# Performance work log

Hardware: AMD Instinct MI355X
Metric: run time of the kernel (lower is better)

The kernel has to match this reference:

```python
import jax, jax.numpy as jnp
import numpy as np

B, S, H, NH = 4, 2048, 1024, 16
HD = H // NH  # head dim 64


def setup_inputs() -> dict:
    key = jax.random.key(0)
    ks = jax.random.split(key, 8)
    s = 1.0 / np.sqrt(H)
    return {
        "hidden_states": jax.random.normal(ks[0], (B, S, H), dtype=jnp.float32),
        "attention_mask": jnp.zeros((B, 1, 1, S), dtype=jnp.float32),
        "Wq": jax.random.normal(ks[1], (H, H), dtype=jnp.float32) * s,
        "bq": jnp.zeros((H,), dtype=jnp.float32),
        "Wk": jax.random.normal(ks[2], (H, H), dtype=jnp.float32) * s,
        "bk": jnp.zeros((H,), dtype=jnp.float32),
        "Wv": jax.random.normal(ks[3], (H, H), dtype=jnp.float32) * s,
        "bv": jnp.zeros((H,), dtype=jnp.float32),
    }


def _split_heads(x):
    # [B,S,H] -> [B,NH,S,HD]
    b, s, _ = x.shape
    return x.reshape(b, s, NH, HD).transpose(0, 2, 1, 3)


def reference(hidden_states, attention_mask, Wq, bq, Wk, bk, Wv, bv):
    q = _split_heads(hidden_states @ Wq.T + bq)
    k = _split_heads(hidden_states @ Wk.T + bk)
    v = _split_heads(hidden_states @ Wv.T + bv)

    qk = jnp.einsum("bhid,bhjd->bhij", q, k)  # [B,NH,S,S]
    seq = q.shape[2]
    causal = jnp.triu(jnp.ones((seq, seq), dtype=bool), 1)  # True above diagonal
    attn_w = jnp.where(causal, -jnp.inf, qk) + attention_mask
    # NOTE: original divides by sqrt(d_k) AFTER masking/adding attention_mask
    probs = jax.nn.softmax(attn_w / jnp.sqrt(jnp.float32(HD)), axis=-1)
    out = jnp.einsum("bhij,bhjd->bhid", probs, v)  # [B,NH,S,HD]
    return out.transpose(0, 2, 1, 3).reshape(hidden_states.shape[0], seq, NH * HD)
```

## Files before the change

### kernel.cpp

```cpp
#include <hip/hip_runtime.h>


#define B_   4
#define S_   2048
#define H_   1024
#define NH_  16
#define HD_  64
#define M_   (B_ * S_)

typedef float          f32x4  __attribute__((ext_vector_type(4)));
typedef short          bf16x8 __attribute__((ext_vector_type(8)));
typedef unsigned short u16x8  __attribute__((ext_vector_type(8)));

__device__ __forceinline__ unsigned short f2bf(float f) {
    unsigned int u = __float_as_uint(f);
    u += 0x7fffu + ((u >> 16) & 1u);
    return (unsigned short)(u >> 16);
}

__device__ __forceinline__ void load16_lds(const unsigned short* g, unsigned short* l) {
    __builtin_amdgcn_global_load_lds(
        (const __attribute__((address_space(1))) unsigned int*)g,
        (__attribute__((address_space(3))) unsigned int*)l, 16, 0, 0);
}

__global__ __launch_bounds__(256) void cast_bf16(
    const float* __restrict__ s0, const float* __restrict__ s1,
    const float* __restrict__ s2, const float* __restrict__ s3,
    unsigned short* __restrict__ d0, unsigned short* __restrict__ d1,
    unsigned short* __restrict__ d2, unsigned short* __restrict__ d3) {
    const int z = blockIdx.y;
    const float* src = (z == 0) ? s0 : (z == 1) ? s1 : (z == 2) ? s2 : s3;
    unsigned short* dst = (z == 0) ? d0 : (z == 1) ? d1 : (z == 2) ? d2 : d3;
    const int n = (z == 0) ? M_ * H_ : H_ * H_;
    int i = (blockIdx.x * 256 + threadIdx.x) * 8;
    if (i + 8 <= n) {
        float4 a = *(const float4*)(src + i);
        float4 b = *(const float4*)(src + i + 4);
        u16x8 o;
        o[0] = f2bf(a.x); o[1] = f2bf(a.y); o[2] = f2bf(a.z); o[3] = f2bf(a.w);
        o[4] = f2bf(b.x); o[5] = f2bf(b.y); o[6] = f2bf(b.z); o[7] = f2bf(b.w);
        *(u16x8*)(dst + i) = o;
    }
}

__global__ __launch_bounds__(256) void qkv_gemm(
    const unsigned short* __restrict__ A,
    const unsigned short* __restrict__ W0, const unsigned short* __restrict__ W1,
    const unsigned short* __restrict__ W2,
    const float* __restrict__ b0, const float* __restrict__ b1,
    const float* __restrict__ b2,
    unsigned short* __restrict__ o0, unsigned short* __restrict__ o1,
    unsigned short* __restrict__ o2) {
    __shared__ unsigned short sA[128 * 64];
    __shared__ unsigned short sB[128 * 64];
    __shared__ unsigned short sT[64 * 136];

    const int t = threadIdx.x;
    const int w = t >> 6, lane = t & 63, quad = lane >> 4, l15 = lane & 15;
    const int bm = blockIdx.x, bn = blockIdx.y, z = blockIdx.z;

    const unsigned short* W = (z == 0) ? W0 : (z == 1) ? W1 : W2;
    const float*        bia = (z == 0) ? b0 : (z == 1) ? b1 : b2;

    const int wm = (w & 1) * 64, wn = (w >> 1) * 64;

    f32x4 acc[4][4];
#pragma unroll
    for (int i = 0; i < 4; ++i)
#pragma unroll
        for (int j = 0; j < 4; ++j) acc[i][j] = f32x4{0.f, 0.f, 0.f, 0.f};

    const int srow = w * 32 + (lane >> 3);
    const int scol = (lane & 7) * 8;
    const unsigned short* Ag = A + (size_t)(bm * 128 + srow) * H_ + scol;
    const unsigned short* Wg = W + (size_t)(bn * 128 + srow) * H_ + scol;
    unsigned short* lA = &sA[w * 32 * 64];
    unsigned short* lB = &sB[w * 32 * 64];

    for (int kt = 0; kt < 16; ++kt) {
        __syncthreads();
#pragma unroll
        for (int c = 0; c < 4; ++c) {
            load16_lds(Ag + kt * 64 + (size_t)c * 8 * H_, lA + c * 512);
            load16_lds(Wg + kt * 64 + (size_t)c * 8 * H_, lB + c * 512);
        }
        __syncthreads();
#pragma unroll
        for (int kk = 0; kk < 64; kk += 32) {
            bf16x8 af[4], bf[4];
#pragma unroll
            for (int mi = 0; mi < 4; ++mi)
                af[mi] = *(const bf16x8*)&sA[(wm + mi * 16 + l15) * 64 + kk + quad * 8];
#pragma unroll
            for (int ni = 0; ni < 4; ++ni)
                bf[ni] = *(const bf16x8*)&sB[(wn + ni * 16 + l15) * 64 + kk + quad * 8];
#pragma unroll
            for (int mi = 0; mi < 4; ++mi)
#pragma unroll
                for (int ni = 0; ni < 4; ++ni)
                    acc[mi][ni] = __builtin_amdgcn_mfma_f32_16x16x32_bf16(
                        af[mi], bf[ni], acc[mi][ni], 0, 0, 0);
        }
    }

    float bvv[4];
#pragma unroll
    for (int ni = 0; ni < 4; ++ni) bvv[ni] = bia[bn * 128 + wn + ni * 16 + l15];

    if (z != 2) {
        unsigned short* outp = (z == 0) ? o0 : o1;
#pragma unroll
        for (int mi = 0; mi < 4; ++mi)
#pragma unroll
            for (int ni = 0; ni < 4; ++ni)
#pragma unroll
                for (int r = 0; r < 4; ++r) {
                    int m = bm * 128 + wm + mi * 16 + quad * 4 + r;
                    int n = bn * 128 + wn + ni * 16 + l15;
                    outp[(size_t)m * H_ + n] = f2bf(acc[mi][ni][r] + bvv[ni]);
                }
    } else {
        const int halfw = w >> 1;
        const int bb = bm >> 4;
        const int s0 = (bm * 128) & 2047;
        for (int half = 0; half < 2; ++half) {
            if (half) __syncthreads();
            if (halfw == half) {
#pragma unroll
                for (int mi = 0; mi < 4; ++mi)
#pragma unroll
                    for (int ni = 0; ni < 4; ++ni)
#pragma unroll
                        for (int r = 0; r < 4; ++r) {
                            int nl = ni * 16 + l15;
                            int m  = wm + mi * 16 + quad * 4 + r;
                            sT[nl * 136 + m] = f2bf(acc[mi][ni][r] + bvv[ni]);
                        }
            }
            __syncthreads();
            {
                int nl = t >> 2, mc = (t & 3) * 32;
                int ng = bn * 128 + half * 64 + nl;
                int hh = ng >> 6, d = ng & 63;
                size_t base = ((size_t)((bb * NH_ + hh) * HD_ + d)) * S_ + s0 + mc;
#pragma unroll
                for (int i = 0; i < 4; ++i)
                    *(u16x8*)(o2 + base + i * 8) = *(const u16x8*)&sT[nl * 136 + mc + i * 8];
            }
        }
    }
}

__global__ __launch_bounds__(256, 3) void attn(
    const unsigned short* __restrict__ qg, const unsigned short* __restrict__ kg,
    const unsigned short* __restrict__ vtg, const float* __restrict__ maskg,
    float* __restrict__ outg) {
    __shared__ unsigned short k_s[2][64 * 68];
    __shared__ unsigned short v_s[2][64 * 68];
    __shared__ unsigned short p_s[4][16 * 68];
    __shared__ float mask_s[2][64];

    const int t = threadIdx.x;
    const int w = t >> 6, lane = t & 63, quad = lane >> 4, l15 = lane & 15;
    const int bx = blockIdx.x;
    const int bh = blockIdx.y;
    const int b = bh >> 4, h = bh & 15;
    const int qa = bx, qb = 31 - bx;

    const int rs_ = t >> 2;
    const int cs_ = (t & 3) * 16;

    const unsigned short* kbase = kg + ((size_t)b * S_ + rs_) * H_ + h * HD_ + cs_;
    const unsigned short* vbase = vtg + ((size_t)bh * HD_ + rs_) * S_ + cs_;

    bf16x8 aqa[2], aqb[2];
    {
        const unsigned short* qpa =
            qg + ((size_t)(b * S_ + qa * 64 + w * 16 + l15)) * H_ + h * HD_ + quad * 8;
        aqa[0] = *(const bf16x8*)qpa;
        aqa[1] = *(const bf16x8*)(qpa + 32);
        const unsigned short* qpb =
            qg + ((size_t)(b * S_ + qb * 64 + w * 16 + l15)) * H_ + h * HD_ + quad * 8;
        aqb[0] = *(const bf16x8*)qpb;
        aqb[1] = *(const bf16x8*)(qpb + 32);
    }

    u16x8 pk0 = *(const u16x8*)kbase, pk1 = *(const u16x8*)(kbase + 8);
    u16x8 pv0 = *(const u16x8*)vbase, pv1 = *(const u16x8*)(vbase + 8);
    float pm = maskg[b * S_ + (t & 63)];

    f32x4 oa[4], ob[4];
    float la[4] = {0.f, 0.f, 0.f, 0.f}, lb[4] = {0.f, 0.f, 0.f, 0.f};
#pragma unroll
    for (int dt = 0; dt < 4; ++dt) {
        oa[dt] = f32x4{0.f, 0.f, 0.f, 0.f};
        ob[dt] = f32x4{0.f, 0.f, 0.f, 0.f};
    }

    const int iga0 = qa * 64 + w * 16 + quad * 4;
    const int igb0 = qb * 64 + w * 16 + quad * 4;

    for (int kt = 0; kt <= qb; ++kt) {
        const int cur = kt & 1;
        *(u16x8*)&k_s[cur][rs_ * 68 + cs_]     = pk0;
        *(u16x8*)&k_s[cur][rs_ * 68 + cs_ + 8] = pk1;
        *(u16x8*)&v_s[cur][rs_ * 68 + cs_]     = pv0;
        *(u16x8*)&v_s[cur][rs_ * 68 + cs_ + 8] = pv1;
        if (t < 64) mask_s[cur][t] = pm;
        if (kt < qb) {
            const unsigned short* kp = kbase + (size_t)(kt + 1) * 64 * H_;
            pk0 = *(const u16x8*)kp; pk1 = *(const u16x8*)(kp + 8);
            const unsigned short* vp = vbase + (kt + 1) * 64;
            pv0 = *(const u16x8*)vp; pv1 = *(const u16x8*)(vp + 8);
            pm = maskg[b * S_ + (kt + 1) * 64 + (t & 63)];
        }
        __syncthreads();

        {
            f32x4 sc[4];
#pragma unroll
            for (int jt = 0; jt < 4; ++jt) sc[jt] = f32x4{0.f, 0.f, 0.f, 0.f};
#pragma unroll
            for (int c = 0; c < 2; ++c)
#pragma unroll
                for (int jt = 0; jt < 4; ++jt) {
                    bf16x8 bk = *(const bf16x8*)&k_s[cur][(jt * 16 + l15) * 68 + c * 32 + quad * 8];
                    sc[jt] = __builtin_amdgcn_mfma_f32_16x16x32_bf16(aqb[c], bk, sc[jt], 0, 0, 0);
                }
            const bool diag = (kt == qb);
#pragma unroll
            for (int r = 0; r < 4; ++r) {
                float ls = 0.f;
#pragma unroll
                for (int jt = 0; jt < 4; ++jt) {
                    float p = __expf((sc[jt][r] + mask_s[cur][jt * 16 + l15]) * 0.125f);
                    if (diag && (kt * 64 + jt * 16 + l15) > (igb0 + r)) p = 0.f;
                    ls += p;
                    unsigned int u = __float_as_uint(p) + 0x8000u;
                    p_s[w][(quad * 4 + r) * 68 + jt * 16 + l15] = (unsigned short)(u >> 16);
                }
                lb[r] += ls;
            }
#pragma unroll
            for (int c = 0; c < 2; ++c) {
                bf16x8 ap = *(const bf16x8*)&p_s[w][l15 * 68 + c * 32 + quad * 8];
#pragma unroll
                for (int dt = 0; dt < 4; ++dt) {
                    bf16x8 bv = *(const bf16x8*)&v_s[cur][(dt * 16 + l15) * 68 + c * 32 + quad * 8];
                    ob[dt] = __builtin_amdgcn_mfma_f32_16x16x32_bf16(ap, bv, ob[dt], 0, 0, 0);
                }
            }
        }
        if (kt <= qa) {
            f32x4 sc[4];
#pragma unroll
            for (int jt = 0; jt < 4; ++jt) sc[jt] = f32x4{0.f, 0.f, 0.f, 0.f};
#pragma unroll
            for (int c = 0; c < 2; ++c)
#pragma unroll
                for (int jt = 0; jt < 4; ++jt) {
                    bf16x8 bk = *(const bf16x8*)&k_s[cur][(jt * 16 + l15) * 68 + c * 32 + quad * 8];
                    sc[jt] = __builtin_amdgcn_mfma_f32_16x16x32_bf16(aqa[c], bk, sc[jt], 0, 0, 0);
                }
            const bool diag = (kt == qa);
#pragma unroll
            for (int r = 0; r < 4; ++r) {
                float ls = 0.f;
#pragma unroll
                for (int jt = 0; jt < 4; ++jt) {
                    float p = __expf((sc[jt][r] + mask_s[cur][jt * 16 + l15]) * 0.125f);
                    if (diag && (kt * 64 + jt * 16 + l15) > (iga0 + r)) p = 0.f;
                    ls += p;
                    unsigned int u = __float_as_uint(p) + 0x8000u;
                    p_s[w][(quad * 4 + r) * 68 + jt * 16 + l15] = (unsigned short)(u >> 16);
                }
                la[r] += ls;
            }
#pragma unroll
            for (int c = 0; c < 2; ++c) {
                bf16x8 ap = *(const bf16x8*)&p_s[w][l15 * 68 + c * 32 + quad * 8];
#pragma unroll
                for (int dt = 0; dt < 4; ++dt) {
                    bf16x8 bv = *(const bf16x8*)&v_s[cur][(dt * 16 + l15) * 68 + c * 32 + quad * 8];
                    oa[dt] = __builtin_amdgcn_mfma_f32_16x16x32_bf16(ap, bv, oa[dt], 0, 0, 0);
                }
            }
        }
    }

#pragma unroll
    for (int r = 0; r < 4; ++r) {
        float sa = la[r], sb = lb[r];
#pragma unroll
        for (int mk = 1; mk <= 8; mk <<= 1) {
            sa += __shfl_xor(sa, mk);
            sb += __shfl_xor(sb, mk);
        }
        la[r] = 1.0f / sa;
        lb[r] = 1.0f / sb;
    }
#pragma unroll
    for (int dt = 0; dt < 4; ++dt)
#pragma unroll
        for (int r = 0; r < 4; ++r) {
            int col = h * HD_ + dt * 16 + l15;
            outg[(size_t)(b * S_ + iga0 + r) * H_ + col] = oa[dt][r] * la[r];
            outg[(size_t)(b * S_ + igb0 + r) * H_ + col] = ob[dt][r] * lb[r];
        }
}

extern "C" void kernel_launch(void* const* d_in, const int* in_sizes, int n_in,
                              void* d_out, int out_size, void* d_ws, size_t ws_size,
                              hipStream_t stream) {
    const float* hs   = (const float*)d_in[0];
    const float* mask = (const float*)d_in[1];
    const float* Wq   = (const float*)d_in[2];
    const float* bq   = (const float*)d_in[3];
    const float* Wk   = (const float*)d_in[4];
    const float* bk   = (const float*)d_in[5];
    const float* Wv   = (const float*)d_in[6];
    const float* bv   = (const float*)d_in[7];
    float* out = (float*)d_out;

    unsigned short* hsb = (unsigned short*)d_ws;
    unsigned short* wqb = hsb + (size_t)M_ * H_;
    unsigned short* wkb = wqb + (size_t)H_ * H_;
    unsigned short* wvb = wkb + (size_t)H_ * H_;
    unsigned short* qb  = wvb + (size_t)H_ * H_;
    unsigned short* kb  = qb  + (size_t)M_ * H_;
    unsigned short* vtb = kb  + (size_t)M_ * H_;

    cast_bf16<<<dim3((M_ * H_) / 2048, 4), 256, 0, stream>>>(
        hs, Wq, Wk, Wv, hsb, wqb, wkb, wvb);

    qkv_gemm<<<dim3(M_ / 128, H_ / 128, 3), 256, 0, stream>>>(
        hsb, wqb, wkb, wvb, bq, bk, bv, qb, kb, vtb);

    attn<<<dim3(16, B_ * NH_), 256, 0, stream>>>(qb, kb, vtb, mask, out);
}
```

Before: 267.7 us.

## Swizzle attention LDS tiles, prescale mask, use exp2 and MFMA priority

The padded stride-68 LDS layout for K, V and P tiles becomes an XOR-swizzled stride-64 layout. This shrinks shared memory and aims to avoid bank conflicts, which together with launch_bounds raised to 4 could allow more resident blocks. The mask is prescaled by log2(e)/8 in the cast kernel and read per lane into registers instead of staged through LDS. The softmax exponent becomes a single fma plus exp2. setprio is raised around the MFMA sections to favour matrix issue across waves. Risks include register pressure under the tighter launch bound, an extra grid slice in the cast kernel, and extra workspace for the scaled mask.

```diff
diff --git a/kernel.cpp b/kernel.cpp
--- a/kernel.cpp
+++ b/kernel.cpp
@@ -8,6 +8,10 @@
 #define HD_  64
 #define M_   (B_ * S_)
 
+#define CEXP 0.18033688011112042f
+
+#define SWZ(row, col) ((col) ^ (((row) & 7) << 3))
+
 typedef float          f32x4  __attribute__((ext_vector_type(4)));
 typedef short          bf16x8 __attribute__((ext_vector_type(8)));
 typedef unsigned short u16x8  __attribute__((ext_vector_type(8)));
@@ -27,13 +31,26 @@
 __global__ __launch_bounds__(256) void cast_bf16(
     const float* __restrict__ s0, const float* __restrict__ s1,
     const float* __restrict__ s2, const float* __restrict__ s3,
+    const float* __restrict__ s4,
     unsigned short* __restrict__ d0, unsigned short* __restrict__ d1,
-    unsigned short* __restrict__ d2, unsigned short* __restrict__ d3) {
+    unsigned short* __restrict__ d2, unsigned short* __restrict__ d3,
+    float* __restrict__ d4) {
     const int z = blockIdx.y;
+    int i = (blockIdx.x * 256 + threadIdx.x) * 8;
+    if (z == 4) {
+        if (i + 8 <= B_ * S_) {
+            float4 a = *(const float4*)(s4 + i);
+            float4 b = *(const float4*)(s4 + i + 4);
+            a.x *= CEXP; a.y *= CEXP; a.z *= CEXP; a.w *= CEXP;
+            b.x *= CEXP; b.y *= CEXP; b.z *= CEXP; b.w *= CEXP;
+            *(float4*)(d4 + i)     = a;
+            *(float4*)(d4 + i + 4) = b;
+        }
+        return;
+    }
     const float* src = (z == 0) ? s0 : (z == 1) ? s1 : (z == 2) ? s2 : s3;
     unsigned short* dst = (z == 0) ? d0 : (z == 1) ? d1 : (z == 2) ? d2 : d3;
     const int n = (z == 0) ? M_ * H_ : H_ * H_;
-    int i = (blockIdx.x * 256 + threadIdx.x) * 8;
     if (i + 8 <= n) {
         float4 a = *(const float4*)(src + i);
         float4 b = *(const float4*)(src + i + 4);
@@ -152,14 +169,13 @@
     }
 }
 
-__global__ __launch_bounds__(256, 3) void attn(
+__global__ __launch_bounds__(256, 4) void attn(
     const unsigned short* __restrict__ qg, const unsigned short* __restrict__ kg,
-    const unsigned short* __restrict__ vtg, const float* __restrict__ maskg,
+    const unsigned short* __restrict__ vtg, const float* __restrict__ mcg,
     float* __restrict__ outg) {
-    __shared__ unsigned short k_s[2][64 * 68];
-    __shared__ unsigned short v_s[2][64 * 68];
-    __shared__ unsigned short p_s[4][16 * 68];
-    __shared__ float mask_s[2][64];
+    __shared__ unsigned short k_s[2][64 * 64];
+    __shared__ unsigned short v_s[2][64 * 64];
+    __shared__ unsigned short p_s[4][16 * 64];
 
     const int t = threadIdx.x;
     const int w = t >> 6, lane = t & 63, quad = lane >> 4, l15 = lane & 15;
@@ -170,9 +186,12 @@
 
     const int rs_ = t >> 2;
     const int cs_ = (t & 3) * 16;
+    const int sc0 = rs_ * 64 + SWZ(rs_, cs_);
+    const int sc1 = rs_ * 64 + SWZ(rs_, cs_ + 8);
 
     const unsigned short* kbase = kg + ((size_t)b * S_ + rs_) * H_ + h * HD_ + cs_;
     const unsigned short* vbase = vtg + ((size_t)bh * HD_ + rs_) * S_ + cs_;
+    const float* mbase = mcg + b * S_ + l15;
 
     bf16x8 aqa[2], aqb[2];
     {
@@ -188,7 +207,9 @@
 
     u16x8 pk0 = *(const u16x8*)kbase, pk1 = *(const u16x8*)(kbase + 8);
     u16x8 pv0 = *(const u16x8*)vbase, pv1 = *(const u16x8*)(vbase + 8);
-    float pm = maskg[b * S_ + (t & 63)];
+    float pmc[4];
+#pragma unroll
+    for (int j = 0; j < 4; ++j) pmc[j] = mbase[j * 16];
 
     f32x4 oa[4], ob[4];
     float la[4] = {0.f, 0.f, 0.f, 0.f}, lb[4] = {0.f, 0.f, 0.f, 0.f};
@@ -203,17 +224,20 @@
 
     for (int kt = 0; kt <= qb; ++kt) {
         const int cur = kt & 1;
-        *(u16x8*)&k_s[cur][rs_ * 68 + cs_]     = pk0;
-        *(u16x8*)&k_s[cur][rs_ * 68 + cs_ + 8] = pk1;
-        *(u16x8*)&v_s[cur][rs_ * 68 + cs_]     = pv0;
-        *(u16x8*)&v_s[cur][rs_ * 68 + cs_ + 8] = pv1;
-        if (t < 64) mask_s[cur][t] = pm;
+        *(u16x8*)&k_s[cur][sc0] = pk0;
+        *(u16x8*)&k_s[cur][sc1] = pk1;
+        *(u16x8*)&v_s[cur][sc0] = pv0;
+        *(u16x8*)&v_s[cur][sc1] = pv1;
+        float mc_[4];
+#pragma unroll
+        for (int j = 0; j < 4; ++j) mc_[j] = pmc[j];
         if (kt < qb) {
             const unsigned short* kp = kbase + (size_t)(kt + 1) * 64 * H_;
             pk0 = *(const u16x8*)kp; pk1 = *(const u16x8*)(kp + 8);
             const unsigned short* vp = vbase + (kt + 1) * 64;
             pv0 = *(const u16x8*)vp; pv1 = *(const u16x8*)(vp + 8);
-            pm = maskg[b * S_ + (kt + 1) * 64 + (t & 63)];
+#pragma unroll
+            for (int j = 0; j < 4; ++j) pmc[j] = mbase[(kt + 1) * 64 + j * 16];
         }
         __syncthreads();
 
@@ -221,71 +245,85 @@
             f32x4 sc[4];
 #pragma unroll
             for (int jt = 0; jt < 4; ++jt) sc[jt] = f32x4{0.f, 0.f, 0.f, 0.f};
+            __builtin_amdgcn_s_setprio(1);
 #pragma unroll
             for (int c = 0; c < 2; ++c)
 #pragma unroll
                 for (int jt = 0; jt < 4; ++jt) {
-                    bf16x8 bk = *(const bf16x8*)&k_s[cur][(jt * 16 + l15) * 68 + c * 32 + quad * 8];
+                    int row = jt * 16 + l15;
+                    bf16x8 bk = *(const bf16x8*)&k_s[cur][row * 64 + SWZ(row, c * 32 + quad * 8)];
                     sc[jt] = __builtin_amdgcn_mfma_f32_16x16x32_bf16(aqb[c], bk, sc[jt], 0, 0, 0);
                 }
+            __builtin_amdgcn_s_setprio(0);
             const bool diag = (kt == qb);
 #pragma unroll
             for (int r = 0; r < 4; ++r) {
                 float ls = 0.f;
+                const int prow = quad * 4 + r;
 #pragma unroll
                 for (int jt = 0; jt < 4; ++jt) {
-                    float p = __expf((sc[jt][r] + mask_s[cur][jt * 16 + l15]) * 0.125f);
+                    float p = __builtin_amdgcn_exp2f(__builtin_fmaf(sc[jt][r], CEXP, mc_[jt]));
                     if (diag && (kt * 64 + jt * 16 + l15) > (igb0 + r)) p = 0.f;
                     ls += p;
                     unsigned int u = __float_as_uint(p) + 0x8000u;
-                    p_s[w][(quad * 4 + r) * 68 + jt * 16 + l15] = (unsigned short)(u >> 16);
+                    p_s[w][prow * 64 + SWZ(prow, jt * 16 + l15)] = (unsigned short)(u >> 16);
                 }
                 lb[r] += ls;
             }
+            __builtin_amdgcn_s_setprio(1);
 #pragma unroll
             for (int c = 0; c < 2; ++c) {
-                bf16x8 ap = *(const bf16x8*)&p_s[w][l15 * 68 + c * 32 + quad * 8];
+                bf16x8 ap = *(const bf16x8*)&p_s[w][l15 * 64 + SWZ(l15, c * 32 + quad * 8)];
 #pragma unroll
                 for (int dt = 0; dt < 4; ++dt) {
-                    bf16x8 bv = *(const bf16x8*)&v_s[cur][(dt * 16 + l15) * 68 + c * 32 + quad * 8];
+                    int row = dt * 16 + l15;
+                    bf16x8 bv = *(const bf16x8*)&v_s[cur][row * 64 + SWZ(row, c * 32 + quad * 8)];
                     ob[dt] = __builtin_amdgcn_mfma_f32_16x16x32_bf16(ap, bv, ob[dt], 0, 0, 0);
                 }
             }
+            __builtin_amdgcn_s_setprio(0);
         }
         if (kt <= qa) {
             f32x4 sc[4];
 #pragma unroll
             for (int jt = 0; jt < 4; ++jt) sc[jt] = f32x4{0.f, 0.f, 0.f, 0.f};
+            __builtin_amdgcn_s_setprio(1);
 #pragma unroll
             for (int c = 0; c < 2; ++c)
 #pragma unroll
                 for (int jt = 0; jt < 4; ++jt) {
-                    bf16x8 bk = *(const bf16x8*)&k_s[cur][(jt * 16 + l15) * 68 + c * 32 + quad * 8];
+                    int row = jt * 16 + l15;
+                    bf16x8 bk = *(const bf16x8*)&k_s[cur][row * 64 + SWZ(row, c * 32 + quad * 8)];
                     sc[jt] = __builtin_amdgcn_mfma_f32_16x16x32_bf16(aqa[c], bk, sc[jt], 0, 0, 0);
                 }
+            __builtin_amdgcn_s_setprio(0);
             const bool diag = (kt == qa);
 #pragma unroll
             for (int r = 0; r < 4; ++r) {
                 float ls = 0.f;
+                const int prow = quad * 4 + r;
 #pragma unroll
                 for (int jt = 0; jt < 4; ++jt) {
-                    float p = __expf((sc[jt][r] + mask_s[cur][jt * 16 + l15]) * 0.125f);
+                    float p = __builtin_amdgcn_exp2f(__builtin_fmaf(sc[jt][r], CEXP, mc_[jt]));
                     if (diag && (kt * 64 + jt * 16 + l15) > (iga0 + r)) p = 0.f;
                     ls += p;
                     unsigned int u = __float_as_uint(p) + 0x8000u;
-                    p_s[w][(quad * 4 + r) * 68 + jt * 16 + l15] = (unsigned short)(u >> 16);
+                    p_s[w][prow * 64 + SWZ(prow, jt * 16 + l15)] = (unsigned short)(u >> 16);
                 }
                 la[r] += ls;
             }
+            __builtin_amdgcn_s_setprio(1);
 #pragma unroll
             for (int c = 0; c < 2; ++c) {
-                bf16x8 ap = *(const bf16x8*)&p_s[w][l15 * 68 + c * 32 + quad * 8];
+                bf16x8 ap = *(const bf16x8*)&p_s[w][l15 * 64 + SWZ(l15, c * 32 + quad * 8)];
 #pragma unroll
                 for (int dt = 0; dt < 4; ++dt) {
-                    bf16x8 bv = *(const bf16x8*)&v_s[cur][(dt * 16 + l15) * 68 + c * 32 + quad * 8];
+                    int row = dt * 16 + l15;
+                    bf16x8 bv = *(const bf16x8*)&v_s[cur][row * 64 + SWZ(row, c * 32 + quad * 8)];
                     oa[dt] = __builtin_amdgcn_mfma_f32_16x16x32_bf16(ap, bv, oa[dt], 0, 0, 0);
                 }
             }
+            __builtin_amdgcn_s_setprio(0);
         }
     }
 
@@ -330,12 +368,13 @@
     unsigned short* qb  = wvb + (size_t)H_ * H_;
     unsigned short* kb  = qb  + (size_t)M_ * H_;
     unsigned short* vtb = kb  + (size_t)M_ * H_;
-
-    cast_bf16<<<dim3((M_ * H_) / 2048, 4), 256, 0, stream>>>(
-        hs, Wq, Wk, Wv, hsb, wqb, wkb, wvb);
+    float*          mcw = (float*)(vtb + (size_t)M_ * H_);
+
+    cast_bf16<<<dim3((M_ * H_) / 2048, 5), 256, 0, stream>>>(
+        hs, Wq, Wk, Wv, mask, hsb, wqb, wkb, wvb, mcw);
 
     qkv_gemm<<<dim3(M_ / 128, H_ / 128, 3), 256, 0, stream>>>(
         hsb, wqb, wkb, wvb, bq, bk, bv, qb, kb, vtb);
 
-    attn<<<dim3(16, B_ * NH_), 256, 0, stream>>>(qb, kb, vtb, mask, out);
-}
+    attn<<<dim3(16, B_ * NH_), 256, 0, stream>>>(qb, kb, vtb, mcw, out);
+}
```

Result: slower. 338.8 us (+26.5%).
